# Kernel optimization log

Measured on AMD Instinct MI355X. Metric: run time of the kernel, lower is better.

The kernel has to match this reference:

```python
import jax, jax.numpy as jnp
import numpy as np

B, S, D, H = 4, 2048, 1024, 16
HD = D // H


def setup_inputs() -> dict:
    key = jax.random.key(0)
    ks = jax.random.split(key, 6)
    s = 1.0 / np.sqrt(D)
    return {
        "x": jax.random.normal(ks[0], (B, S, D), dtype=jnp.float32),
        "Wq": jax.random.normal(ks[1], (D, D), dtype=jnp.float32) * s,
        "Wk": jax.random.normal(ks[2], (D, D), dtype=jnp.float32) * s,
        "Wv": jax.random.normal(ks[3], (D, D), dtype=jnp.float32) * s,
        "Wo": jax.random.normal(ks[4], (D, D), dtype=jnp.float32) * s,
        "bo": jnp.zeros((D,), dtype=jnp.float32),
    }


def reference(x, Wq, Wk, Wv, Wo, bo):
    b, n, d = x.shape
    # QKV projections (torch Linear: x @ W.T, but weights here are stored as [d_in, d_out])
    q = (x @ Wq).reshape(b, n, H, HD).transpose(0, 2, 1, 3)  # [b,h,n,hd]
    k = (x @ Wk).reshape(b, n, H, HD).transpose(0, 2, 1, 3)
    v = (x @ Wv).reshape(b, n, H, HD).transpose(0, 2, 1, 3)
    scores = jnp.einsum("bhqd,bhkd->bhqk", q, k) / np.sqrt(HD)
    causal = jnp.tril(jnp.ones((n, n), dtype=bool))  # True = keep
    scores = jnp.where(causal, scores, -jnp.inf)
    attn = jax.nn.softmax(scores, axis=-1)
    ctx = jnp.einsum("bhqk,bhkd->bhqd", attn, v)
    ctx = ctx.transpose(0, 2, 1, 3).reshape(b, n, d)
    return ctx @ Wo + bo
```

## Files before the change

### kernel.cpp

```cpp
#include <hip/hip_runtime.h>
#include <hip/hip_bf16.h>

typedef __bf16 bf16;
typedef __bf16 bf16x8 __attribute__((ext_vector_type(8)));
typedef float f32x4 __attribute__((ext_vector_type(4)));

static constexpr int Bn = 4, Sn = 2048, Dn = 1024, Hn = 16, HDn = 64;
static constexpr int Mn = Bn * Sn;

__device__ __forceinline__ void gload_lds16(const void* g, void* l) {
  __builtin_amdgcn_global_load_lds(
      (const __attribute__((address_space(1))) unsigned int*)g,
      (__attribute__((address_space(3))) unsigned int*)l, 16, 0, 0);
}

__global__ void cvt_x_kernel(const float* __restrict__ x, bf16* __restrict__ xb, int n8) {
  int i = blockIdx.x * blockDim.x + threadIdx.x;
  if (i >= n8) return;
  const float4* p = reinterpret_cast<const float4*>(x) + (size_t)i * 2;
  float4 a = p[0], b = p[1];
  bf16x8 v;
  v[0] = (bf16)a.x; v[1] = (bf16)a.y; v[2] = (bf16)a.z; v[3] = (bf16)a.w;
  v[4] = (bf16)b.x; v[5] = (bf16)b.y; v[6] = (bf16)b.z; v[7] = (bf16)b.w;
  *(reinterpret_cast<bf16x8*>(xb) + i) = v;
}

struct alignas(8) B4 { bf16 e[4]; };

__global__ void transpose_w_kernel(const float* __restrict__ W0, const float* __restrict__ W1,
                                   const float* __restrict__ W2, const float* __restrict__ W3,
                                   bf16* __restrict__ WtQKV, bf16* __restrict__ Wot) {
  __shared__ bf16 tile[64][65];
  const int which = blockIdx.z;
  const float* W = (which == 0) ? W0 : (which == 1) ? W1 : (which == 2) ? W2 : W3;
  bf16* out = (which < 3) ? (WtQKV + (size_t)which * 1024 * 1024) : Wot;
  const int k0 = blockIdx.y * 64, n0 = blockIdx.x * 64;
  const int t = threadIdx.x;
  const int tr = t >> 4, tc = (t & 15) * 4;
#pragma unroll
  for (int rr = 0; rr < 4; ++rr) {
    const int row = rr * 16 + tr;
    float4 v = *reinterpret_cast<const float4*>(&W[(size_t)(k0 + row) * 1024 + n0 + tc]);
    tile[row][tc + 0] = (bf16)v.x; tile[row][tc + 1] = (bf16)v.y;
    tile[row][tc + 2] = (bf16)v.z; tile[row][tc + 3] = (bf16)v.w;
  }
  __syncthreads();
#pragma unroll
  for (int rr = 0; rr < 4; ++rr) {
    const int row = rr * 16 + tr;
    B4 o;
#pragma unroll
    for (int j = 0; j < 4; ++j) o.e[j] = tile[tc + j][row];
    *reinterpret_cast<B4*>(&out[(size_t)(n0 + row) * 1024 + k0 + tc]) = o;
  }
}

template <int MODE>
__global__ __launch_bounds__(256, 2)
void gemm_kernel(const bf16* __restrict__ A, const bf16* __restrict__ Bt,
                 float* __restrict__ Co, const float* __restrict__ bias,
                 bf16* __restrict__ Qo, bf16* __restrict__ Ko, bf16* __restrict__ Vto) {
  __shared__ bf16 Al[2][128 * 64];
  __shared__ bf16 Bl[2][128 * 64];
  const int tid = threadIdx.x;
  const int lane = tid & 63;
  const int wv = tid >> 6;
  const int wm = wv >> 1, wn = wv & 1;
  const int lr = lane & 15, lg = lane >> 4;
  const int m0 = blockIdx.y * 128, n0 = blockIdx.x * 128;

  int soff[4];
  const bf16* srcA[4];
  const bf16* srcB[4];
#pragma unroll
  for (int it = 0; it < 4; ++it) {
    const int elem = it * 2048 + tid * 8;
    const int row = elem >> 6;
    const int g = (elem >> 3) & 7;
    const int gs = g ^ (row & 7);
    soff[it] = elem;
    srcA[it] = A + (size_t)(m0 + row) * 1024 + gs * 8;
    srcB[it] = Bt + (size_t)(n0 + row) * 1024 + gs * 8;
  }

  f32x4 acc[4][4] = {};

#pragma unroll
  for (int it = 0; it < 4; ++it) {
    gload_lds16(srcA[it], (bf16*)&Al[0][0] + soff[it]);
    gload_lds16(srcB[it], (bf16*)&Bl[0][0] + soff[it]);
  }
  __syncthreads();

  for (int ks = 0; ks < 16; ++ks) {
    const int cur = ks & 1;
    if (ks + 1 < 16) {
      const int kn = (ks + 1) * 64;
#pragma unroll
      for (int it = 0; it < 4; ++it) {
        gload_lds16(srcA[it] + kn, (bf16*)&Al[cur ^ 1][0] + soff[it]);
        gload_lds16(srcB[it] + kn, (bf16*)&Bl[cur ^ 1][0] + soff[it]);
      }
    }
    const bf16* AlF = Al[cur];
    const bf16* BlF = Bl[cur];
#pragma unroll
    for (int kk = 0; kk < 2; ++kk) {
      bf16x8 af[4], bfr[4];
#pragma unroll
      for (int i = 0; i < 4; ++i) {
        const int row = wm * 64 + i * 16 + lr;
        af[i] = *reinterpret_cast<const bf16x8*>(AlF + row * 64 + (((kk * 4 + lg) ^ (row & 7)) << 3));
      }
#pragma unroll
      for (int i = 0; i < 4; ++i) {
        const int row = wn * 64 + i * 16 + lr;
        bfr[i] = *reinterpret_cast<const bf16x8*>(BlF + row * 64 + (((kk * 4 + lg) ^ (row & 7)) << 3));
      }
#pragma unroll
      for (int mi = 0; mi < 4; ++mi)
#pragma unroll
        for (int ni = 0; ni < 4; ++ni)
          acc[mi][ni] = __builtin_amdgcn_mfma_f32_16x16x32_bf16(af[mi], bfr[ni], acc[mi][ni], 0, 0, 0);
    }
    __syncthreads();
  }

  const int mrow = lg * 4;
  if (MODE == 0) {
    const int w = n0 >> 10;
    const int nl0 = n0 & 1023;
    if (w == 2) {
      const int b = m0 >> 11;
      const int s0 = (m0 & 2047) + wm * 64 + mrow;
#pragma unroll
      for (int ni = 0; ni < 4; ++ni) {
        const int nl = nl0 + wn * 64 + ni * 16 + lr;
        const int h = nl >> 6, hd = nl & 63;
        bf16* vbase = Vto + ((size_t)(b * 16 + h) * 64 + hd) * 2048;
#pragma unroll
        for (int mi = 0; mi < 4; ++mi) {
          B4 o;
#pragma unroll
          for (int i = 0; i < 4; ++i) o.e[i] = (bf16)acc[mi][ni][i];
          *reinterpret_cast<B4*>(&vbase[s0 + mi * 16]) = o;
        }
      }
    } else {
      const float fs = (w == 0) ? 0.18033688011112042f : 1.0f;
#pragma unroll
      for (int ni = 0; ni < 4; ++ni) {
        const int nl = nl0 + wn * 64 + ni * 16 + lr;
        const int h = nl >> 6, hd = nl & 63;
        bf16* dst = (w == 0) ? Qo : Ko;
#pragma unroll
        for (int mi = 0; mi < 4; ++mi) {
#pragma unroll
          for (int i = 0; i < 4; ++i) {
            const int m_g = m0 + wm * 64 + mi * 16 + mrow + i;
            const int b = m_g >> 11, s = m_g & 2047;
            dst[((size_t)(b * 16 + h) * 2048 + s) * 64 + hd] = (bf16)(acc[mi][ni][i] * fs);
          }
        }
      }
    }
  } else {
#pragma unroll
    for (int ni = 0; ni < 4; ++ni) {
      const int n_g = n0 + wn * 64 + ni * 16 + lr;
      const float bv = bias[n_g];
#pragma unroll
      for (int mi = 0; mi < 4; ++mi) {
#pragma unroll
        for (int i = 0; i < 4; ++i) {
          const int m_g = m0 + wm * 64 + mi * 16 + mrow + i;
          Co[(size_t)m_g * 1024 + n_g] = acc[mi][ni][i] + bv;
        }
      }
    }
  }
}

__device__ __forceinline__ void attn_tile(const bf16* __restrict__ KlF,
                                          const bf16* __restrict__ VlF,
                                          bf16* __restrict__ PlW,
                                          const bf16x8 (&aq)[2], f32x4 (&acc)[4],
                                          float& lst, int kv0, int qrow, bool domask,
                                          int lr, int lg) {
  f32x4 sc[4] = {};
#pragma unroll
  for (int kk = 0; kk < 2; ++kk) {
    bf16x8 ak[4];
#pragma unroll
    for (int ni = 0; ni < 4; ++ni) {
      const int row = ni * 16 + lr;
      ak[ni] = *reinterpret_cast<const bf16x8*>(KlF + row * 64 + (((kk * 4 + lg) ^ (row & 7)) << 3));
    }
    __builtin_amdgcn_s_setprio(1);
#pragma unroll
    for (int ni = 0; ni < 4; ++ni)
      sc[ni] = __builtin_amdgcn_mfma_f32_16x16x32_bf16(ak[ni], aq[kk], sc[ni], 0, 0, 0);
    __builtin_amdgcn_s_setprio(0);
  }
  float p[4][4];
  float rs = 0.f;
#pragma unroll
  for (int ni = 0; ni < 4; ++ni)
#pragma unroll
    for (int r = 0; r < 4; ++r) {
      float pv = __builtin_amdgcn_exp2f(sc[ni][r]);
      if (domask && (kv0 + ni * 16 + lg * 4 + r > qrow)) pv = 0.f;
      p[ni][r] = pv;
      rs += pv;
    }
  rs += __shfl_xor(rs, 16);
  rs += __shfl_xor(rs, 32);
  lst += rs;
#pragma unroll
  for (int ni = 0; ni < 4; ++ni)
#pragma unroll
    for (int tt = 0; tt < 2; ++tt) {
      const int key = ni * 16 + lg * 4 + 2 * tt;
      union { bf16 bb[2]; unsigned int u; } pk;
      pk.bb[0] = (bf16)p[ni][2 * tt];
      pk.bb[1] = (bf16)p[ni][2 * tt + 1];
      const int off = lr * 128 + (((key >> 3) ^ (lr & 7)) << 4) + (key & 7) * 2;
      *reinterpret_cast<unsigned int*>(reinterpret_cast<char*>(PlW) + off) = pk.u;
    }
#pragma unroll
  for (int kk = 0; kk < 2; ++kk) {
    bf16x8 ap = *reinterpret_cast<const bf16x8*>(PlW + lr * 64 + (((kk * 4 + lg) ^ (lr & 7)) << 3));
    bf16x8 bv[4];
#pragma unroll
    for (int ni = 0; ni < 4; ++ni) {
      const int row = ni * 16 + lr;
      bv[ni] = *reinterpret_cast<const bf16x8*>(VlF + row * 64 + (((kk * 4 + lg) ^ (row & 7)) << 3));
    }
    __builtin_amdgcn_s_setprio(1);
#pragma unroll
    for (int ni = 0; ni < 4; ++ni)
      acc[ni] = __builtin_amdgcn_mfma_f32_16x16x32_bf16(ap, bv[ni], acc[ni], 0, 0, 0);
    __builtin_amdgcn_s_setprio(0);
  }
}

__global__ __launch_bounds__(256, 4)
void attn_kernel(const bf16* __restrict__ Q, const bf16* __restrict__ K,
                 const bf16* __restrict__ Vt, bf16* __restrict__ ctx) {
  __shared__ bf16 Kl[2][4096];
  __shared__ bf16 Vl[2][4096];
  __shared__ bf16 Pl[4][1024];
  const int tid = threadIdx.x, lane = tid & 63, wv = tid >> 6;
  const int lr = lane & 15, lg = lane >> 4, lk = lg * 8;
  const int bh = blockIdx.y;
  const int pi = blockIdx.x;
  const bf16* Qh = Q + (size_t)bh * Sn * 64;
  const bf16* Kh = K + (size_t)bh * Sn * 64;
  const bf16* Vh = Vt + (size_t)bh * 64 * (size_t)Sn;
  const int b = bh >> 4, h = bh & 15;
  bf16* PlW = Pl[wv];

  const int e0 = tid * 8, e1 = 2048 + tid * 8;
  const int r0 = e0 >> 6, r1 = e1 >> 6;
  const int gs0 = ((e0 >> 3) & 7) ^ (r0 & 7), gs1 = ((e1 >> 3) & 7) ^ (r1 & 7);
  const bf16* srcK0 = Kh + r0 * 64 + gs0 * 8;
  const bf16* srcK1 = Kh + r1 * 64 + gs1 * 8;
  const bf16* srcV0 = Vh + (size_t)r0 * Sn + gs0 * 8;
  const bf16* srcV1 = Vh + (size_t)r1 * Sn + gs1 * 8;

  const int tA = 31 - pi, tB = pi;
  const int qwA = tA * 64 + wv * 16, qwB = tB * 64 + wv * 16;
  const int qrowA = qwA + lr, qrowB = qwB + lr;

  bf16x8 aqA[2], aqB[2];
#pragma unroll
  for (int kk = 0; kk < 2; ++kk) {
    aqA[kk] = *reinterpret_cast<const bf16x8*>(&Qh[(size_t)(qwA + lr) * 64 + kk * 32 + lk]);
    aqB[kk] = *reinterpret_cast<const bf16x8*>(&Qh[(size_t)(qwB + lr) * 64 + kk * 32 + lk]);
  }

  f32x4 accA[4] = {}, accB[4] = {};
  float lstA = 0.f, lstB = 0.f;

  gload_lds16(srcK0, &Kl[0][e0]);
  gload_lds16(srcK1, &Kl[0][e1]);
  gload_lds16(srcV0, &Vl[0][e0]);
  gload_lds16(srcV1, &Vl[0][e1]);
  __syncthreads();

  for (int t = 0; t <= tA; ++t) {
    const int cur = t & 1;
    if (t < tA) {
      const int kvn = (t + 1) * 64;
      gload_lds16(srcK0 + kvn * 64, &Kl[cur ^ 1][e0]);
      gload_lds16(srcK1 + kvn * 64, &Kl[cur ^ 1][e1]);
      gload_lds16(srcV0 + kvn, &Vl[cur ^ 1][e0]);
      gload_lds16(srcV1 + kvn, &Vl[cur ^ 1][e1]);
    }
    const bf16* KlF = Kl[cur];
    const bf16* VlF = Vl[cur];
    attn_tile(KlF, VlF, PlW, aqA, accA, lstA, t * 64, qrowA, t == tA, lr, lg);
    if (t <= tB)
      attn_tile(KlF, VlF, PlW, aqB, accB, lstB, t * 64, qrowB, t == tB, lr, lg);
    __syncthreads();
  }

  {
    const float inv = 1.f / lstA;
    float invd[4];
#pragma unroll
    for (int i = 0; i < 4; ++i) invd[i] = __shfl(inv, lg * 4 + i);
#pragma unroll
    for (int i = 0; i < 4; ++i) {
      const int row = qwA + lg * 4 + i;
#pragma unroll
      for (int ni = 0; ni < 4; ++ni)
        ctx[(((size_t)b * Sn + row) * 16 + h) * 64 + ni * 16 + lr] = (bf16)(accA[ni][i] * invd[i]);
    }
  }
  {
    const float inv = 1.f / lstB;
    float invd[4];
#pragma unroll
    for (int i = 0; i < 4; ++i) invd[i] = __shfl(inv, lg * 4 + i);
#pragma unroll
    for (int i = 0; i < 4; ++i) {
      const int row = qwB + lg * 4 + i;
#pragma unroll
      for (int ni = 0; ni < 4; ++ni)
        ctx[(((size_t)b * Sn + row) * 16 + h) * 64 + ni * 16 + lr] = (bf16)(accB[ni][i] * invd[i]);
    }
  }
}

extern "C" void kernel_launch(void* const* d_in, const int* in_sizes, int n_in,
                              void* d_out, int out_size, void* d_ws, size_t ws_size,
                              hipStream_t stream) {
  const float* x = (const float*)d_in[0];
  const float* Wq = (const float*)d_in[1];
  const float* Wk = (const float*)d_in[2];
  const float* Wv = (const float*)d_in[3];
  const float* Wo = (const float*)d_in[4];
  const float* bo = (const float*)d_in[5];

  char* ws = (char*)d_ws;
  bf16* xb    = (bf16*)(ws);
  bf16* WtQKV = (bf16*)(ws + 0x1000000);
  bf16* Wot   = (bf16*)(ws + 0x1600000);
  bf16* Qb    = (bf16*)(ws + 0x1800000);
  bf16* Kb    = (bf16*)(ws + 0x2800000);
  bf16* Vtb   = (bf16*)(ws + 0x3800000);
  bf16* ctx   = xb;

  cvt_x_kernel<<<dim3(Mn * Dn / 8 / 256), dim3(256), 0, stream>>>(x, xb, Mn * Dn / 8);
  transpose_w_kernel<<<dim3(16, 16, 4), dim3(256), 0, stream>>>(Wq, Wk, Wv, Wo, WtQKV, Wot);
  gemm_kernel<0><<<dim3(24, 64), dim3(256), 0, stream>>>(xb, WtQKV, nullptr, nullptr, Qb, Kb, Vtb);
  attn_kernel<<<dim3(16, 64), dim3(256), 0, stream>>>(Qb, Kb, Vtb, ctx);
  gemm_kernel<1><<<dim3(8, 64), dim3(256), 0, stream>>>(ctx, Wot, (float*)d_out, bo,
                                                        nullptr, nullptr, nullptr);
}
```

Baseline: 175.6 us.

## Pass attention probabilities between lanes with shuffles instead of LDS staging

Removes the per-wave LDS buffer used to re-layout P from the QK^T accumulator layout into the PV MFMA operand layout. P is now exchanged through cross-lane shuffles, and the PV MFMA operands are swapped so the output is transposed, which lets the epilogue write four contiguous bf16 per lane without the shuffle of the inverse row sum. This cuts LDS writes and reads and frees LDS, at the cost of 16 shuffles plus selects per tile. The epilogue relies on a B4 type assumed to be defined elsewhere.

```diff
diff --git a/kernel.cpp b/kernel.cpp
--- a/kernel.cpp
+++ b/kernel.cpp
@@ -183,10 +183,9 @@
 
 __device__ __forceinline__ void attn_tile(const bf16* __restrict__ KlF,
                                           const bf16* __restrict__ VlF,
-                                          bf16* __restrict__ PlW,
                                           const bf16x8 (&aq)[2], f32x4 (&acc)[4],
                                           float& lst, int kv0, int qrow, bool domask,
-                                          int lr, int lg) {
+                                          int lr, int lg, int src0, int src1) {
   f32x4 sc[4] = {};
 #pragma unroll
   for (int kk = 0; kk < 2; ++kk) {
@@ -216,20 +215,27 @@
   rs += __shfl_xor(rs, 16);
   rs += __shfl_xor(rs, 32);
   lst += rs;
+  unsigned int pk[4][2];
 #pragma unroll
   for (int ni = 0; ni < 4; ++ni)
 #pragma unroll
     for (int tt = 0; tt < 2; ++tt) {
-      const int key = ni * 16 + lg * 4 + 2 * tt;
-      union { bf16 bb[2]; unsigned int u; } pk;
-      pk.bb[0] = (bf16)p[ni][2 * tt];
-      pk.bb[1] = (bf16)p[ni][2 * tt + 1];
-      const int off = lr * 128 + (((key >> 3) ^ (lr & 7)) << 4) + (key & 7) * 2;
-      *reinterpret_cast<unsigned int*>(reinterpret_cast<char*>(PlW) + off) = pk.u;
-    }
+      union { bf16 bb[2]; unsigned int u; } c;
+      c.bb[0] = (bf16)p[ni][2 * tt];
+      c.bb[1] = (bf16)p[ni][2 * tt + 1];
+      pk[ni][tt] = c.u;
+    }
+  const bool sel = (lg & 2) != 0;
 #pragma unroll
   for (int kk = 0; kk < 2; ++kk) {
-    bf16x8 ap = *reinterpret_cast<const bf16x8*>(PlW + lr * 64 + (((kk * 4 + lg) ^ (lr & 7)) << 3));
+    union { unsigned int u[4]; bf16x8 v; } ap;
+#pragma unroll
+    for (int w = 0; w < 4; ++w) {
+      const int srcl = (w < 2) ? src0 : src1;
+      const unsigned int lo = (unsigned int)__shfl((int)pk[2 * kk][w & 1], srcl);
+      const unsigned int hi = (unsigned int)__shfl((int)pk[2 * kk + 1][w & 1], srcl);
+      ap.u[w] = sel ? hi : lo;
+    }
     bf16x8 bv[4];
 #pragma unroll
     for (int ni = 0; ni < 4; ++ni) {
@@ -239,7 +245,7 @@
     __builtin_amdgcn_s_setprio(1);
 #pragma unroll
     for (int ni = 0; ni < 4; ++ni)
-      acc[ni] = __builtin_amdgcn_mfma_f32_16x16x32_bf16(ap, bv[ni], acc[ni], 0, 0, 0);
+      acc[ni] = __builtin_amdgcn_mfma_f32_16x16x32_bf16(bv[ni], ap.v, acc[ni], 0, 0, 0);
     __builtin_amdgcn_s_setprio(0);
   }
 }
@@ -249,7 +255,6 @@
                  const bf16* __restrict__ Vt, bf16* __restrict__ ctx) {
   __shared__ bf16 Kl[2][4096];
   __shared__ bf16 Vl[2][4096];
-  __shared__ bf16 Pl[4][1024];
   const int tid = threadIdx.x, lane = tid & 63, wv = tid >> 6;
   const int lr = lane & 15, lg = lane >> 4, lk = lg * 8;
   const int bh = blockIdx.y;
@@ -258,7 +263,8 @@
   const bf16* Kh = K + (size_t)bh * Sn * 64;
   const bf16* Vh = Vt + (size_t)bh * 64 * (size_t)Sn;
   const int b = bh >> 4, h = bh & 15;
-  bf16* PlW = Pl[wv];
+  const int src0 = lr + 32 * (lg & 1);
+  const int src1 = src0 + 16;
 
   const int e0 = tid * 8, e1 = 2048 + tid * 8;
   const int r0 = e0 >> 6, r1 = e1 >> 6;
@@ -299,36 +305,32 @@
     }
     const bf16* KlF = Kl[cur];
     const bf16* VlF = Vl[cur];
-    attn_tile(KlF, VlF, PlW, aqA, accA, lstA, t * 64, qrowA, t == tA, lr, lg);
+    attn_tile(KlF, VlF, aqA, accA, lstA, t * 64, qrowA, t == tA, lr, lg, src0, src1);
     if (t <= tB)
-      attn_tile(KlF, VlF, PlW, aqB, accB, lstB, t * 64, qrowB, t == tB, lr, lg);
+      attn_tile(KlF, VlF, aqB, accB, lstB, t * 64, qrowB, t == tB, lr, lg, src0, src1);
     __syncthreads();
   }
 
   {
     const float inv = 1.f / lstA;
-    float invd[4];
-#pragma unroll
-    for (int i = 0; i < 4; ++i) invd[i] = __shfl(inv, lg * 4 + i);
-#pragma unroll
-    for (int i = 0; i < 4; ++i) {
-      const int row = qwA + lg * 4 + i;
-#pragma unroll
-      for (int ni = 0; ni < 4; ++ni)
-        ctx[(((size_t)b * Sn + row) * 16 + h) * 64 + ni * 16 + lr] = (bf16)(accA[ni][i] * invd[i]);
+    bf16* cbase = ctx + (((size_t)b * Sn + qwA + lr) * 16 + h) * 64;
+#pragma unroll
+    for (int ni = 0; ni < 4; ++ni) {
+      B4 o;
+#pragma unroll
+      for (int r = 0; r < 4; ++r) o.e[r] = (bf16)(accA[ni][r] * inv);
+      *reinterpret_cast<B4*>(cbase + ni * 16 + lg * 4) = o;
     }
   }
   {
     const float inv = 1.f / lstB;
-    float invd[4];
-#pragma unroll
-    for (int i = 0; i < 4; ++i) invd[i] = __shfl(inv, lg * 4 + i);
-#pragma unroll
-    for (int i = 0; i < 4; ++i) {
-      const int row = qwB + lg * 4 + i;
-#pragma unroll
-      for (int ni = 0; ni < 4; ++ni)
-        ctx[(((size_t)b * Sn + row) * 16 + h) * 64 + ni * 16 + lr] = (bf16)(accB[ni][i] * invd[i]);
+    bf16* cbase = ctx + (((size_t)b * Sn + qwB + lr) * 16 + h) * 64;
+#pragma unroll
+    for (int ni = 0; ni < 4; ++ni) {
+      B4 o;
+#pragma unroll
+      for (int r = 0; r < 4; ++r) o.e[r] = (bf16)(accB[ni][r] * inv);
+      *reinterpret_cast<B4*>(cbase + ni * 16 + lg * 4) = o;
     }
   }
 }
```

Measured after the change: 182.8 us. 1.04x slower.
